# Optimization experiments

Hardware: AMD Instinct MI355X
Metric: run time of the kernel (lower is better)

The kernel has to match this reference:

```python
import jax, jax.numpy as jnp
import numpy as np

NEG_BIG = -9e15
ALPHA = 0.2  # leakyrelu negative slope

N, F_IN, F_OUT = 8192, 512, 64


def setup_inputs() -> dict:
    key = jax.random.key(0)
    k1, k2, k3, k4 = jax.random.split(key, 4)
    input = jax.random.normal(k1, (N, F_IN), dtype=jnp.float32)
    adj = jax.random.randint(k2, (N, N), 0, 2, dtype=jnp.int32)
    W = jax.random.normal(k3, (F_IN, F_OUT), dtype=jnp.float32) * 0.05
    a = jax.random.normal(k4, (2 * F_OUT, 1), dtype=jnp.float32) * 0.1
    return {"input": input, "adj": adj, "W": W, "a": a}


def reference(input, adj, W, a):
    # h: [N, F_out]
    h = input @ W
    # The original builds a_input[i,j] = concat(h_i, h_j) and dots with a.
    # Decompose: e_ij = leakyrelu(h_i @ a_src + h_j @ a_dst) -- identical math,
    # avoids the N*N*2F intermediate.
    a_src = a[:F_OUT, 0]  # [F_out]
    a_dst = a[F_OUT:, 0]  # [F_out]
    s_src = h @ a_src     # [N]
    s_dst = h @ a_dst     # [N]
    e = jax.nn.leaky_relu(s_src[:, None] + s_dst[None, :], negative_slope=ALPHA)  # [N, N]
    masked = jnp.where(adj > 0, e, jnp.float32(NEG_BIG))
    attention = jax.nn.softmax(masked, axis=1)  # dropout omitted (eval mode)
    h_prime = attention @ h  # [N, F_out]
    return jax.nn.elu(h_prime)  # concat=True
```

## Files before the change

kernel.cpp:

```cpp
#include <hip/hip_runtime.h>
#include <hip/hip_bf16.h>

namespace {
constexpr int kN    = 8192;
constexpr int kFin  = 512;
constexpr int kFout = 64;
constexpr float kAlpha = 0.2f;
constexpr int kJSplit = 4;
constexpr int kJLen   = kN / kJSplit;
constexpr int kChunks = kJLen / 128;

using bf16x8 = __attribute__((ext_vector_type(8))) short;
using f32x4  = __attribute__((ext_vector_type(4))) float;

__device__ __forceinline__ unsigned short f2bf(float x) {
  return __builtin_bit_cast(unsigned short, __float2bfloat16(x));
}
__device__ __forceinline__ float lrelu(float x) {
  return fmaxf(x, kAlpha * x);
}
__device__ __forceinline__ unsigned int fkey(float x) {
  unsigned int b = __float_as_uint(x);
  return (b & 0x80000000u) ? ~b : (b | 0x80000000u);
}
__device__ __forceinline__ float fdec(unsigned int k) {
  return (k & 0x80000000u) ? __uint_as_float(k ^ 0x80000000u) : __uint_as_float(~k);
}
}

__global__ __launch_bounds__(256) void k_wt(const float* __restrict__ W,
                                            float* __restrict__ WT,
                                            unsigned int* __restrict__ Smax_u) {
  const int gid = blockIdx.x * 256 + threadIdx.x;
  if (gid == 0) *Smax_u = 0u;
  const int k = gid >> 6, f = gid & 63;
  WT[(size_t)f * kFin + k] = W[gid];
}

__global__ __launch_bounds__(256) void k_linear(
    const float* __restrict__ X, const float* __restrict__ WT, const float* __restrict__ A,
    unsigned short* __restrict__ hTf, float* __restrict__ s_src, float* __restrict__ s_dst,
    unsigned int* __restrict__ Smax_u)
{
  const int t = threadIdx.x;
  const int wv = t >> 6, f = t & 63;
  const int i0 = blockIdx.x * 16;

  __shared__ float Xlds[16 * kFin];
  __shared__ unsigned short h_sm[16][64];
  __shared__ float red[4];

  {
    const float4* Xg = (const float4*)(X + (size_t)i0 * kFin);
    float4* Xl = (float4*)Xlds;
    float4 v0 = Xg[t +   0], v1 = Xg[t + 256], v2 = Xg[t +  512], v3 = Xg[t +  768];
    float4 v4 = Xg[t +1024], v5 = Xg[t +1280], v6 = Xg[t + 1536], v7 = Xg[t + 1792];
    Xl[t +    0] = v0; Xl[t +  256] = v1; Xl[t +  512] = v2; Xl[t +  768] = v3;
    Xl[t + 1024] = v4; Xl[t + 1280] = v5; Xl[t + 1536] = v6; Xl[t + 1792] = v7;
  }
  __syncthreads();

  const int r0l = wv * 4;
  const float* w0 = WT + (size_t)f * kFin;
  float acc0 = 0.f, acc1 = 0.f, acc2 = 0.f, acc3 = 0.f;
  float4 wb0 = *(const float4*)(w0 + 0);
  float4 wb1 = *(const float4*)(w0 + 4);
  const float* xr = Xlds + r0l * kFin;
  for (int k = 0; k < kFin; k += 4) {
    const float4 wc = (k & 4) ? wb1 : wb0;
    if (k + 8 < kFin) {
      const float4 wn = *(const float4*)(w0 + k + 8);
      if (k & 4) wb1 = wn; else wb0 = wn;
    }
    const float4 xa = *(const float4*)(xr + k);
    const float4 xb = *(const float4*)(xr + kFin + k);
    const float4 xc = *(const float4*)(xr + 2 * kFin + k);
    const float4 xd = *(const float4*)(xr + 3 * kFin + k);
#pragma unroll
    for (int j = 0; j < 4; ++j) {
      const float wk = ((const float*)&wc)[j];
      acc0 = fmaf(((const float*)&xa)[j], wk, acc0);
      acc1 = fmaf(((const float*)&xb)[j], wk, acc1);
      acc2 = fmaf(((const float*)&xc)[j], wk, acc2);
      acc3 = fmaf(((const float*)&xd)[j], wk, acc3);
    }
  }

  const float asrc = A[f], adst = A[kFout + f];
  float accs[4] = {acc0, acc1, acc2, acc3};
  float dmax = -3.4e38f;
#pragma unroll
  for (int r = 0; r < 4; ++r) {
    float vs = accs[r] * asrc;
    float vd = accs[r] * adst;
#pragma unroll
    for (int off = 32; off > 0; off >>= 1) {
      vs += __shfl_xor(vs, off, 64);
      vd += __shfl_xor(vd, off, 64);
    }
    if (f == 0) {
      s_src[i0 + r0l + r] = vs;
      s_dst[i0 + r0l + r] = vd;
      dmax = fmaxf(dmax, vd);
    }
    h_sm[r0l + r][f] = f2bf(accs[r]);
  }
  if (f == 0) red[wv] = dmax;
  __syncthreads();
  if (t == 0) {
    float m = fmaxf(fmaxf(red[0], red[1]), fmaxf(red[2], red[3]));
    atomicMax(Smax_u, fkey(m));
  }

  if (t < 128) {
    const int jblk = i0 >> 5, half = (i0 >> 4) & 1;
    const int w = t >> 5, li = t & 31;
    const int lane = half * 32 + li;
    const int ql = li >> 4, fcol = w * 16 + (li & 15);
    bf16x8 v;
#pragma unroll
    for (int e = 0; e < 8; ++e) v[e] = (short)h_sm[ql * 8 + e][fcol];
    *(bf16x8*)(hTf + (size_t)jblk * 2048 + w * 512 + (size_t)lane * 8) = v;
  }
}

__global__ __launch_bounds__(256) void k_attn(
    const int* __restrict__ adj, const unsigned short* __restrict__ hTf,
    const float* __restrict__ s_src, const float* __restrict__ s_dst,
    const unsigned int* __restrict__ Smax_u, float* __restrict__ accp,
    float* __restrict__ lp)
{
  const int t = threadIdx.x;
  const int wv = t >> 6, lane = t & 63;
  const int b = blockIdx.x;
  const int i0 = (b >> 2) * 16;
  const int jbase = (b & 3) * kJLen;
  const int mrow = lane & 15, quad = lane >> 4;

  __shared__ float Racc[4][16][64];
  __shared__ float Rl[4][16];

  const float S = fdec(*Smax_u);
  const float ssrc = s_src[i0 + mrow];
  const float mr = lrelu(ssrc + S);

  float l_acc = 0.f;
  f32x4 acc0 = {0.f,0.f,0.f,0.f}, acc1 = {0.f,0.f,0.f,0.f};
  f32x4 acc2 = {0.f,0.f,0.f,0.f}, acc3 = {0.f,0.f,0.f,0.f};

  const int4*   aptr = (const int4*)(adj + (size_t)(i0 + mrow) * kN + jbase + wv * 32 + quad * 8);
  const float4* dptr = (const float4*)(s_dst + jbase + wv * 32 + quad * 8);
  const unsigned short* hbase = hTf + ((size_t)(jbase >> 5) + wv) * 2048 + (size_t)lane * 8;

  int4   A0a = aptr[0],  A1a = aptr[1];
  float4 D0a = dptr[0],  D1a = dptr[1];
  int4   A0b = aptr[32], A1b = aptr[33];
  float4 D0b = dptr[32], D1b = dptr[33];

  auto phase = [&](int c, int4& A0, int4& A1, float4& D0, float4& D1)
      __attribute__((always_inline)) {
    float pv[8];
    {
      const int* aa = (const int*)&A0;
      const float* dd = (const float*)&D0;
#pragma unroll
      for (int j = 0; j < 4; ++j) {
        const float e = lrelu(ssrc + dd[j]);
        pv[j] = aa[j] > 0 ? __expf(e - mr) : 0.f;
      }
      aa = (const int*)&A1; dd = (const float*)&D1;
#pragma unroll
      for (int j = 0; j < 4; ++j) {
        const float e = lrelu(ssrc + dd[j]);
        pv[4 + j] = aa[j] > 0 ? __expf(e - mr) : 0.f;
      }
    }
    bf16x8 ps;
#pragma unroll
    for (int j = 0; j < 8; ++j) {
      l_acc += pv[j];
      ps[j] = (short)f2bf(pv[j]);
    }

    const unsigned short* hc = hbase + (size_t)c * 8192;
    const uint4 hv0 = *(const uint4*)(hc + 0 * 512);
    const uint4 hv1 = *(const uint4*)(hc + 1 * 512);
    const uint4 hv2 = *(const uint4*)(hc + 2 * 512);
    const uint4 hv3 = *(const uint4*)(hc + 3 * 512);

    if (c + 2 < kChunks) {
      A0 = aptr[(c + 2) * 32]; A1 = aptr[(c + 2) * 32 + 1];
      D0 = dptr[(c + 2) * 32]; D1 = dptr[(c + 2) * 32 + 1];
    }

    acc0 = __builtin_amdgcn_mfma_f32_16x16x32_bf16(ps, __builtin_bit_cast(bf16x8, hv0), acc0, 0, 0, 0);
    acc1 = __builtin_amdgcn_mfma_f32_16x16x32_bf16(ps, __builtin_bit_cast(bf16x8, hv1), acc1, 0, 0, 0);
    acc2 = __builtin_amdgcn_mfma_f32_16x16x32_bf16(ps, __builtin_bit_cast(bf16x8, hv2), acc2, 0, 0, 0);
    acc3 = __builtin_amdgcn_mfma_f32_16x16x32_bf16(ps, __builtin_bit_cast(bf16x8, hv3), acc3, 0, 0, 0);
  };

  for (int c = 0; c < kChunks; c += 2) {
    phase(c,     A0a, A1a, D0a, D1a);
    phase(c + 1, A0b, A1b, D0b, D1b);
  }

  float lv = l_acc;
  lv += __shfl_xor(lv, 16, 64);
  lv += __shfl_xor(lv, 32, 64);
  if (quad == 0) Rl[wv][mrow] = lv;

#pragma unroll
  for (int reg = 0; reg < 4; ++reg) {
    Racc[wv][quad * 4 + reg][0 * 16 + mrow] = acc0[reg];
    Racc[wv][quad * 4 + reg][1 * 16 + mrow] = acc1[reg];
    Racc[wv][quad * 4 + reg][2 * 16 + mrow] = acc2[reg];
    Racc[wv][quad * 4 + reg][3 * 16 + mrow] = acc3[reg];
  }
  __syncthreads();

  float* ab = accp + (size_t)b * 16 * 64;
  const int rr = t >> 4, ff = t & 15;
#pragma unroll
  for (int s = 0; s < 4; ++s) {
    const int f = s * 16 + ff;
    ab[rr * 64 + f] = Racc[0][rr][f] + Racc[1][rr][f] + Racc[2][rr][f] + Racc[3][rr][f];
  }
  if (t < 16) lp[(size_t)b * 16 + t] = Rl[0][t] + Rl[1][t] + Rl[2][t] + Rl[3][t];
}

__global__ __launch_bounds__(256) void k_comb(const float* __restrict__ accp,
                                              const float* __restrict__ lp,
                                              float* __restrict__ out)
{
  const int gid = blockIdx.x * 256 + threadIdx.x;
  const int i = gid >> 6, f = gid & 63;
  const int ib = i >> 4, il = i & 15;
  const int b0 = ib * kJSplit;
  float a = 0.f, l = 0.f;
#pragma unroll
  for (int q = 0; q < kJSplit; ++q) {
    a += accp[((size_t)(b0 + q) * 16 + il) * 64 + f];
    l += lp[(size_t)(b0 + q) * 16 + il];
  }
  float v = a / l;
  v = v > 0.f ? v : __expf(v) - 1.f;
  out[gid] = v;
}

extern "C" void kernel_launch(void* const* d_in, const int* in_sizes, int n_in,
                              void* d_out, int out_size, void* d_ws, size_t ws_size,
                              hipStream_t stream) {
  const float* X   = (const float*)d_in[0];
  const int*   adj = (const int*)d_in[1];
  const float* W   = (const float*)d_in[2];
  const float* A   = (const float*)d_in[3];
  float* out = (float*)d_out;

  char* ws = (char*)d_ws;
  unsigned short* hTf = (unsigned short*)ws;  ws += (size_t)kN * kFout * 2;
  float* WT    = (float*)ws;                  ws += (size_t)kFout * kFin * 4;
  float* s_src = (float*)ws;                  ws += kN * 4;
  float* s_dst = (float*)ws;                  ws += kN * 4;
  unsigned int* Smax_u = (unsigned int*)ws;   ws += 256;
  float* accp  = (float*)ws;                  ws += (size_t)(kN / 16) * kJSplit * 16 * 64 * 4;
  float* lp    = (float*)ws;

  k_wt    <<<kFin * kFout / 256, 256, 0, stream>>>(W, WT, Smax_u);
  k_linear<<<kN / 16, 256, 0, stream>>>(X, WT, A, hTf, s_src, s_dst, Smax_u);
  k_attn  <<<(kN / 16) * kJSplit, 256, 0, stream>>>(adj, hTf, s_src, s_dst, Smax_u, accp, lp);
  k_comb  <<<kN * kFout / 256, 256, 0, stream>>>(accp, lp, out);
}
```

Baseline: 423.5 us.

## Pack adjacency into bitmask in fused prep kernel; attention reads bits

A new prep kernel fuses the linear projection with a pass that compresses the int32 adjacency matrix into a 64-bit-per-word bitmask using wave ballots. The attention kernel then reads one mask word per group of columns instead of streaming int4 adjacency loads inside its MFMA loop. The W-transpose kernel is removed: the projection reads X and W straight from global memory instead of staging X in LDS, and a memset resets the max. The goal is to take the large adjacency stream off the latency-sensitive attention loop. The cost is that the full adjacency read now runs as its own pass before attention, and the projection gives up its LDS reuse of X.

```diff
diff --git a/kernel.cpp b/kernel.cpp
--- a/kernel.cpp
+++ b/kernel.cpp
@@ -28,57 +28,48 @@
 }
 }
 
-__global__ __launch_bounds__(256) void k_wt(const float* __restrict__ W,
-                                            float* __restrict__ WT,
-                                            unsigned int* __restrict__ Smax_u) {
-  const int gid = blockIdx.x * 256 + threadIdx.x;
-  if (gid == 0) *Smax_u = 0u;
-  const int k = gid >> 6, f = gid & 63;
-  WT[(size_t)f * kFin + k] = W[gid];
-}
-
-__global__ __launch_bounds__(256) void k_linear(
-    const float* __restrict__ X, const float* __restrict__ WT, const float* __restrict__ A,
-    unsigned short* __restrict__ hTf, float* __restrict__ s_src, float* __restrict__ s_dst,
+__global__ __launch_bounds__(256) void k_prep(
+    const int* __restrict__ adj, const float* __restrict__ X,
+    const float* __restrict__ W, const float* __restrict__ A,
+    unsigned long long* __restrict__ mask, unsigned short* __restrict__ hTf,
+    float* __restrict__ s_src, float* __restrict__ s_dst,
     unsigned int* __restrict__ Smax_u)
 {
   const int t = threadIdx.x;
-  const int wv = t >> 6, f = t & 63;
+  const int wv = t >> 6, lane = t & 63;
+
+  if (blockIdx.x >= 512) {
+    const int row = (blockIdx.x - 512) * 4 + wv;
+    const int* __restrict__ ar = adj + (size_t)row * kN;
+    unsigned long long* __restrict__ mr = mask + (size_t)row * 128;
+#pragma unroll 8
+    for (int it = 0; it < 128; ++it) {
+      const int v = ar[it * 64 + lane];
+      const unsigned long long bal = __ballot(v > 0);
+      if (lane == (it & 63)) mr[it] = bal;
+    }
+    return;
+  }
+
+  const int wvu = __builtin_amdgcn_readfirstlane(wv);
+  const int f = lane;
   const int i0 = blockIdx.x * 16;
-
-  __shared__ float Xlds[16 * kFin];
+  const int r0l = wvu * 4;
+
   __shared__ unsigned short h_sm[16][64];
   __shared__ float red[4];
 
-  {
-    const float4* Xg = (const float4*)(X + (size_t)i0 * kFin);
-    float4* Xl = (float4*)Xlds;
-    float4 v0 = Xg[t +   0], v1 = Xg[t + 256], v2 = Xg[t +  512], v3 = Xg[t +  768];
-    float4 v4 = Xg[t +1024], v5 = Xg[t +1280], v6 = Xg[t + 1536], v7 = Xg[t + 1792];
-    Xl[t +    0] = v0; Xl[t +  256] = v1; Xl[t +  512] = v2; Xl[t +  768] = v3;
-    Xl[t + 1024] = v4; Xl[t + 1280] = v5; Xl[t + 1536] = v6; Xl[t + 1792] = v7;
-  }
-  __syncthreads();
-
-  const int r0l = wv * 4;
-  const float* w0 = WT + (size_t)f * kFin;
+  const float* x0 = X + (size_t)(i0 + r0l) * kFin;
   float acc0 = 0.f, acc1 = 0.f, acc2 = 0.f, acc3 = 0.f;
-  float4 wb0 = *(const float4*)(w0 + 0);
-  float4 wb1 = *(const float4*)(w0 + 4);
-  const float* xr = Xlds + r0l * kFin;
+#pragma unroll 2
   for (int k = 0; k < kFin; k += 4) {
-    const float4 wc = (k & 4) ? wb1 : wb0;
-    if (k + 8 < kFin) {
-      const float4 wn = *(const float4*)(w0 + k + 8);
-      if (k & 4) wb1 = wn; else wb0 = wn;
-    }
-    const float4 xa = *(const float4*)(xr + k);
-    const float4 xb = *(const float4*)(xr + kFin + k);
-    const float4 xc = *(const float4*)(xr + 2 * kFin + k);
-    const float4 xd = *(const float4*)(xr + 3 * kFin + k);
+    const float4 xa = *(const float4*)(x0 + k);
+    const float4 xb = *(const float4*)(x0 + kFin + k);
+    const float4 xc = *(const float4*)(x0 + 2 * kFin + k);
+    const float4 xd = *(const float4*)(x0 + 3 * kFin + k);
 #pragma unroll
     for (int j = 0; j < 4; ++j) {
-      const float wk = ((const float*)&wc)[j];
+      const float wk = W[(k + j) * kFout + f];
       acc0 = fmaf(((const float*)&xa)[j], wk, acc0);
       acc1 = fmaf(((const float*)&xb)[j], wk, acc1);
       acc2 = fmaf(((const float*)&xc)[j], wk, acc2);
@@ -105,7 +96,7 @@
     }
     h_sm[r0l + r][f] = f2bf(accs[r]);
   }
-  if (f == 0) red[wv] = dmax;
+  if (f == 0) red[wvu] = dmax;
   __syncthreads();
   if (t == 0) {
     float m = fmaxf(fmaxf(red[0], red[1]), fmaxf(red[2], red[3]));
@@ -115,17 +106,18 @@
   if (t < 128) {
     const int jblk = i0 >> 5, half = (i0 >> 4) & 1;
     const int w = t >> 5, li = t & 31;
-    const int lane = half * 32 + li;
+    const int ln = half * 32 + li;
     const int ql = li >> 4, fcol = w * 16 + (li & 15);
     bf16x8 v;
 #pragma unroll
     for (int e = 0; e < 8; ++e) v[e] = (short)h_sm[ql * 8 + e][fcol];
-    *(bf16x8*)(hTf + (size_t)jblk * 2048 + w * 512 + (size_t)lane * 8) = v;
+    *(bf16x8*)(hTf + (size_t)jblk * 2048 + w * 512 + (size_t)ln * 8) = v;
   }
 }
 
 __global__ __launch_bounds__(256) void k_attn(
-    const int* __restrict__ adj, const unsigned short* __restrict__ hTf,
+    const unsigned long long* __restrict__ mask,
+    const unsigned short* __restrict__ hTf,
     const float* __restrict__ s_src, const float* __restrict__ s_dst,
     const unsigned int* __restrict__ Smax_u, float* __restrict__ accp,
     float* __restrict__ lp)
@@ -134,7 +126,8 @@
   const int wv = t >> 6, lane = t & 63;
   const int b = blockIdx.x;
   const int i0 = (b >> 2) * 16;
-  const int jbase = (b & 3) * kJLen;
+  const int q = b & 3;
+  const int jbase = q * kJLen;
   const int mrow = lane & 15, quad = lane >> 4;
 
   __shared__ float Racc[4][16][64];
@@ -148,31 +141,33 @@
   f32x4 acc0 = {0.f,0.f,0.f,0.f}, acc1 = {0.f,0.f,0.f,0.f};
   f32x4 acc2 = {0.f,0.f,0.f,0.f}, acc3 = {0.f,0.f,0.f,0.f};
 
-  const int4*   aptr = (const int4*)(adj + (size_t)(i0 + mrow) * kN + jbase + wv * 32 + quad * 8);
+  const unsigned long long* mptr =
+      mask + (size_t)(i0 + mrow) * 128 + (jbase >> 6) + (wv >> 1);
+  const int sh = (wv & 1) * 32 + quad * 8;
   const float4* dptr = (const float4*)(s_dst + jbase + wv * 32 + quad * 8);
-  const unsigned short* hbase = hTf + ((size_t)(jbase >> 5) + wv) * 2048 + (size_t)lane * 8;
-
-  int4   A0a = aptr[0],  A1a = aptr[1];
+  const unsigned short* hbase =
+      hTf + ((size_t)(jbase >> 5) + wv) * 2048 + (size_t)lane * 8;
+
+  unsigned long long m0 = mptr[0], m1 = mptr[2], m2 = mptr[4], m3 = mptr[6];
   float4 D0a = dptr[0],  D1a = dptr[1];
-  int4   A0b = aptr[32], A1b = aptr[33];
   float4 D0b = dptr[32], D1b = dptr[33];
 
-  auto phase = [&](int c, int4& A0, int4& A1, float4& D0, float4& D1)
+  auto phase = [&](int c, unsigned long long mw, float4& D0, float4& D1)
       __attribute__((always_inline)) {
+    const unsigned int B = (unsigned int)(mw >> sh) & 0xffu;
     float pv[8];
     {
-      const int* aa = (const int*)&A0;
       const float* dd = (const float*)&D0;
 #pragma unroll
       for (int j = 0; j < 4; ++j) {
         const float e = lrelu(ssrc + dd[j]);
-        pv[j] = aa[j] > 0 ? __expf(e - mr) : 0.f;
+        pv[j] = (B >> j) & 1u ? __expf(e - mr) : 0.f;
       }
-      aa = (const int*)&A1; dd = (const float*)&D1;
+      dd = (const float*)&D1;
 #pragma unroll
       for (int j = 0; j < 4; ++j) {
         const float e = lrelu(ssrc + dd[j]);
-        pv[4 + j] = aa[j] > 0 ? __expf(e - mr) : 0.f;
+        pv[4 + j] = (B >> (4 + j)) & 1u ? __expf(e - mr) : 0.f;
       }
     }
     bf16x8 ps;
@@ -189,7 +184,6 @@
     const uint4 hv3 = *(const uint4*)(hc + 3 * 512);
 
     if (c + 2 < kChunks) {
-      A0 = aptr[(c + 2) * 32]; A1 = aptr[(c + 2) * 32 + 1];
       D0 = dptr[(c + 2) * 32]; D1 = dptr[(c + 2) * 32 + 1];
     }
 
@@ -199,9 +193,17 @@
     acc3 = __builtin_amdgcn_mfma_f32_16x16x32_bf16(ps, __builtin_bit_cast(bf16x8, hv3), acc3, 0, 0, 0);
   };
 
-  for (int c = 0; c < kChunks; c += 2) {
-    phase(c,     A0a, A1a, D0a, D1a);
-    phase(c + 1, A0b, A1b, D0b, D1b);
+  for (int g = 0; g < 4; ++g) {
+    unsigned long long n0 = 0, n1 = 0, n2 = 0, n3 = 0;
+    if (g < 3) {
+      n0 = mptr[g * 8 + 8]; n1 = mptr[g * 8 + 10];
+      n2 = mptr[g * 8 + 12]; n3 = mptr[g * 8 + 14];
+    }
+    phase(g * 4 + 0, m0, D0a, D1a);
+    phase(g * 4 + 1, m1, D0b, D1b);
+    phase(g * 4 + 2, m2, D0a, D1a);
+    phase(g * 4 + 3, m3, D0b, D1b);
+    m0 = n0; m1 = n1; m2 = n2; m3 = n3;
   }
 
   float lv = l_acc;
@@ -222,8 +224,8 @@
   const int rr = t >> 4, ff = t & 15;
 #pragma unroll
   for (int s = 0; s < 4; ++s) {
-    const int f = s * 16 + ff;
-    ab[rr * 64 + f] = Racc[0][rr][f] + Racc[1][rr][f] + Racc[2][rr][f] + Racc[3][rr][f];
+    const int fc = s * 16 + ff;
+    ab[rr * 64 + fc] = Racc[0][rr][fc] + Racc[1][rr][fc] + Racc[2][rr][fc] + Racc[3][rr][fc];
   }
   if (t < 16) lp[(size_t)b * 16 + t] = Rl[0][t] + Rl[1][t] + Rl[2][t] + Rl[3][t];
 }
@@ -238,9 +240,9 @@
   const int b0 = ib * kJSplit;
   float a = 0.f, l = 0.f;
 #pragma unroll
-  for (int q = 0; q < kJSplit; ++q) {
-    a += accp[((size_t)(b0 + q) * 16 + il) * 64 + f];
-    l += lp[(size_t)(b0 + q) * 16 + il];
+  for (int qq = 0; qq < kJSplit; ++qq) {
+    a += accp[((size_t)(b0 + qq) * 16 + il) * 64 + f];
+    l += lp[(size_t)(b0 + qq) * 16 + il];
   }
   float v = a / l;
   v = v > 0.f ? v : __expf(v) - 1.f;
@@ -257,16 +259,16 @@
   float* out = (float*)d_out;
 
   char* ws = (char*)d_ws;
+  unsigned long long* mask = (unsigned long long*)ws;  ws += (size_t)kN * 128 * 8;
   unsigned short* hTf = (unsigned short*)ws;  ws += (size_t)kN * kFout * 2;
-  float* WT    = (float*)ws;                  ws += (size_t)kFout * kFin * 4;
   float* s_src = (float*)ws;                  ws += kN * 4;
   float* s_dst = (float*)ws;                  ws += kN * 4;
   unsigned int* Smax_u = (unsigned int*)ws;   ws += 256;
   float* accp  = (float*)ws;                  ws += (size_t)(kN / 16) * kJSplit * 16 * 64 * 4;
   float* lp    = (float*)ws;
 
-  k_wt    <<<kFin * kFout / 256, 256, 0, stream>>>(W, WT, Smax_u);
-  k_linear<<<kN / 16, 256, 0, stream>>>(X, WT, A, hTf, s_src, s_dst, Smax_u);
-  k_attn  <<<(kN / 16) * kJSplit, 256, 0, stream>>>(adj, hTf, s_src, s_dst, Smax_u, accp, lp);
-  k_comb  <<<kN * kFout / 256, 256, 0, stream>>>(accp, lp, out);
-}
+  hipMemsetAsync(Smax_u, 0, 4, stream);
+  k_prep <<<512 + kN / 4, 256, 0, stream>>>(adj, X, W, A, mask, hTf, s_src, s_dst, Smax_u);
+  k_attn <<<(kN / 16) * kJSplit, 256, 0, stream>>>(mask, hTf, s_src, s_dst, Smax_u, accp, lp);
+  k_comb <<<kN * kFout / 256, 256, 0, stream>>>(accp, lp, out);
+}
```

Measured after the change: 474.5 us. +12.0%, slower.
